# Optimization experiments

Measured on AMD Instinct MI355X. Metric: run time of the kernel, lower is better.

The kernel has to match this reference:

```python
import jax, jax.numpy as jnp
import numpy as np

N, E, F_IN, G = 100000, 1600000, 128, 64
H1, H2, H3 = 64, 32, 16


def _xavier(key, fan_in, fan_out):
    lim = np.sqrt(6.0 / (fan_in + fan_out))
    return jax.random.uniform(key, (fan_in, fan_out), jnp.float32, -lim, lim)


def setup_inputs() -> dict:
    key = jax.random.key(0)
    ks = jax.random.split(key, 16)
    x = jax.random.normal(ks[0], (N, F_IN), jnp.float32)
    edge_index = jax.random.randint(ks[1], (2, E), 0, N, dtype=jnp.int32)
    batch = jnp.sort(jax.random.randint(ks[2], (N,), 0, G, dtype=jnp.int32))
    d = {
        "x": x,
        "W1": _xavier(ks[3], F_IN, H1), "b1": jnp.zeros((H1,), jnp.float32),
        "W2": _xavier(ks[4], H1, H2), "b2": jnp.zeros((H2,), jnp.float32),
        "W3": _xavier(ks[5], H2, H3), "b3": jnp.zeros((H3,), jnp.float32),
        "g1": jnp.ones((H1,), jnp.float32), "be1": jnp.zeros((H1,), jnp.float32),
        "g2": jnp.ones((H2,), jnp.float32), "be2": jnp.zeros((H2,), jnp.float32),
        "g3": jnp.ones((H3,), jnp.float32), "be3": jnp.zeros((H3,), jnp.float32),
        "attn_w": _xavier(ks[6], 3 * H3, 3), "attn_b": jnp.zeros((3,), jnp.float32),
        "fc1_w": _xavier(ks[7], H3, H3), "fc1_b": jnp.zeros((H3,), jnp.float32),
        "fc2_w": _xavier(ks[8], H3, H3 // 2), "fc2_b": jnp.zeros((H3 // 2,), jnp.float32),
        "out_w": _xavier(ks[9], H3 // 2, 1), "out_b": jnp.zeros((1,), jnp.float32),
        "edge_index": edge_index,
        "batch": batch,
        "num_graphs": G,
    }
    return d


def _lrelu(z):
    return jnp.where(z > 0, z, 0.1 * z)


def _bn(h, gamma, beta, eps=1e-5):
    # BatchNorm1d forward with batch statistics (biased variance), as torch training-mode math
    m = jnp.mean(h, axis=0)
    v = jnp.mean(jnp.square(h - m), axis=0)
    return (h - m) * jax.lax.rsqrt(v + eps) * gamma + beta


def reference(x, W1, b1, W2, b2, W3, b3, g1, be1, g2, be2, g3, be3,
              attn_w, attn_b, fc1_w, fc1_b, fc2_w, fc2_b, out_w, out_b,
              edge_index, batch, num_graphs):
    src, dst = edge_index[0], edge_index[1]
    n = x.shape[0]
    # GCN degree with self-loops: deg[i] = 1 + #incoming edges
    deg = jax.ops.segment_sum(jnp.ones((src.shape[0],), x.dtype), dst, num_segments=n) + 1.0
    dis = jax.lax.rsqrt(deg)                      # deg^-1/2, [N]
    enorm = dis[src] * dis[dst]                   # per-edge norm, [E]
    selfw = dis * dis                             # self-loop norm, [N]

    def gcn(h, W, b):
        hw = h @ W                                # [N, H]
        agg = jax.ops.segment_sum(hw[src] * enorm[:, None], dst, num_segments=n)
        return agg + selfw[:, None] * hw + b

    x1 = _lrelu(_bn(gcn(x, W1, b1), g1, be1))     # dropout = identity (eval)
    x2 = _lrelu(_bn(gcn(x1, W2, b2), g2, be2))    # residual skipped: 64 != 32
    x3 = _lrelu(_bn(gcn(x2, W3, b3), g3, be3))    # residual skipped: 32 != 16

    # multi-pool over graphs
    ones_n = jnp.ones((n,), x.dtype)
    counts = jax.ops.segment_sum(ones_n, batch, num_segments=num_graphs)  # [G]
    x_sum = jax.ops.segment_sum(x3, batch, num_segments=num_graphs)       # [G, H3]
    x_mean = x_sum / jnp.maximum(counts, 1.0)[:, None]
    x_max = jax.ops.segment_max(x3, batch, num_segments=num_graphs)

    pooled = jnp.concatenate([x_mean, x_max, x_sum], axis=1)              # [G, 3*H3]
    aw = jax.nn.softmax(pooled @ attn_w + attn_b, axis=1)                 # [G, 3]
    xg = aw[:, 0:1] * x_mean + aw[:, 1:2] * x_max + aw[:, 2:3] * x_sum    # [G, H3]

    xg = _lrelu(xg @ fc1_w + fc1_b)
    xg = _lrelu(xg @ fc2_w + fc2_b)
    out = jax.nn.sigmoid(xg @ out_w + out_b)                              # [G, 1]
    return out
```

## Files before the change

### kernel.cpp

```cpp
#include <hip/hip_runtime.h>

#define GG 64
#define SREP 32
typedef unsigned long long ull;
typedef unsigned short u16;

__device__ __forceinline__ u16 f2b(float x) {
    unsigned u = __float_as_uint(x);
    return (u16)((u + 0x7FFFu + ((u >> 16) & 1u)) >> 16);
}

__device__ __forceinline__ void add8(const uint4 q, float* acc) {
    acc[0] += __uint_as_float(q.x << 16);
    acc[1] += __uint_as_float(q.x & 0xFFFF0000u);
    acc[2] += __uint_as_float(q.y << 16);
    acc[3] += __uint_as_float(q.y & 0xFFFF0000u);
    acc[4] += __uint_as_float(q.z << 16);
    acc[5] += __uint_as_float(q.z & 0xFFFF0000u);
    acc[6] += __uint_as_float(q.w << 16);
    acc[7] += __uint_as_float(q.w & 0xFFFF0000u);
}

__global__ void k_hist(const int* __restrict__ dst, int* __restrict__ cnt, int E) {
    int e = blockIdx.x * blockDim.x + threadIdx.x;
    if (e < E) atomicAdd(&cnt[dst[e]], 1);
}

__global__ void k_dis(const int* __restrict__ cnt, float* __restrict__ dis, int n) {
    int i = blockIdx.x * blockDim.x + threadIdx.x;
    if (i < n) dis[i] = rsqrtf((float)cnt[i] + 1.0f);
}

__global__ void k_scanA(const int* __restrict__ cnt, int* __restrict__ rp,
                        int* __restrict__ bsum, int n) {
    __shared__ int s[256];
    int i = blockIdx.x * 256 + threadIdx.x;
    int v = (i < n) ? cnt[i] : 0;
    s[threadIdx.x] = v;
    __syncthreads();
    for (int off = 1; off < 256; off <<= 1) {
        int t = (threadIdx.x >= off) ? s[threadIdx.x - off] : 0;
        __syncthreads();
        s[threadIdx.x] += t;
        __syncthreads();
    }
    if (i < n) rp[i] = s[threadIdx.x] - v;
    if (threadIdx.x == 255) bsum[blockIdx.x] = s[255];
}

__global__ void k_scanB(int* __restrict__ bsum, int nb) {
    __shared__ int s[512];
    int v = (threadIdx.x < nb) ? bsum[threadIdx.x] : 0;
    s[threadIdx.x] = v;
    __syncthreads();
    for (int off = 1; off < 512; off <<= 1) {
        int t = (threadIdx.x >= off) ? s[threadIdx.x - off] : 0;
        __syncthreads();
        s[threadIdx.x] += t;
        __syncthreads();
    }
    if (threadIdx.x < nb) bsum[threadIdx.x] = s[threadIdx.x] - v;
}

__global__ void k_scanC(int* __restrict__ rp, const int* __restrict__ bsum,
                        int* __restrict__ cursor, int n, int E) {
    int i = blockIdx.x * 256 + threadIdx.x;
    if (i < n) {
        int r = rp[i] + bsum[blockIdx.x];
        rp[i] = r;
        cursor[i] = r;
    }
    if (i == 0) rp[n] = E;
}

__global__ __launch_bounds__(256) void k_scatter(const int* __restrict__ src,
                                                 const int* __restrict__ dst,
                                                 int* __restrict__ cursor,
                                                 ull* __restrict__ epack, int E, int n) {
    const int part = blockIdx.x & 7;
    const int nblk = gridDim.x >> 3;
    const int bser = blockIdx.x >> 3;
    const int lo = (int)(((long long)part * n) >> 3);
    const int hi = (part == 7) ? n : (int)(((long long)(part + 1) * n) >> 3);
    for (int e = bser * 256 + threadIdx.x; e < E; e += nblk * 256) {
        int d = dst[e];
        if (d >= lo && d < hi) {
            int s = src[e];
            int pos = atomicAdd(&cursor[d], 1);
            epack[pos] = (ull)(unsigned)s;
        }
    }
}

template <int FIN, int FOUT, bool BN>
__global__ __launch_bounds__(256) void k_mm(const float* __restrict__ h,
                                            const float* __restrict__ W,
                                            const float* __restrict__ dis,
                                            const float* __restrict__ stats,
                                            const float* __restrict__ gma,
                                            const float* __restrict__ bta,
                                            u16* __restrict__ hw, int n) {
    constexpr int FX  = FOUT / 4;
    constexpr int TY  = 256 / FX;
    constexpr int NT  = TY * 4;
    constexpr int LDA = FIN + ((FOUT == 64) ? 2 : 1);
    __shared__ float sA[NT * LDA];
    __shared__ float sW[FIN * FOUT];
    __shared__ float sSc[FIN], sSh[FIN];

    if (BN && threadIdx.x < FIN) {
        int f = threadIdx.x;
        float s = 0.f, q = 0.f;
        #pragma unroll 8
        for (int r = 0; r < SREP; ++r) {
            s += stats[(r << 7) + f];
            q += stats[(r << 7) + 64 + f];
        }
        float inv_n = 1.0f / (float)n;
        float m = s * inv_n;
        float var = fmaxf(q * inv_n - m * m, 0.f);
        float sc = rsqrtf(var + 1e-5f) * gma[f];
        sSc[f] = sc;
        sSh[f] = bta[f] - m * sc;
    }
    for (int i = threadIdx.x; i < FIN * FOUT / 4; i += 256)
        ((float4*)sW)[i] = ((const float4*)W)[i];
    if (BN) __syncthreads();

    const int node0 = blockIdx.x * NT;
    constexpr int LD4 = NT * FIN / 4 / 256;
    #pragma unroll
    for (int i = 0; i < LD4; ++i) {
        int idx4 = i * 256 + threadIdx.x;
        int row = idx4 / (FIN / 4);
        int c4  = idx4 % (FIN / 4);
        int gn  = node0 + row;
        float4 v = make_float4(0.f, 0.f, 0.f, 0.f);
        if (gn < n) v = ((const float4*)(h + (long long)gn * FIN))[c4];
        if (BN) {
            int f = c4 * 4;
            float t;
            t = fmaf(v.x, sSc[f + 0], sSh[f + 0]); v.x = t > 0.f ? t : 0.1f * t;
            t = fmaf(v.y, sSc[f + 1], sSh[f + 1]); v.y = t > 0.f ? t : 0.1f * t;
            t = fmaf(v.z, sSc[f + 2], sSh[f + 2]); v.z = t > 0.f ? t : 0.1f * t;
            t = fmaf(v.w, sSc[f + 3], sSh[f + 3]); v.w = t > 0.f ? t : 0.1f * t;
        }
        float* p = &sA[row * LDA + c4 * 4];
        p[0] = v.x; p[1] = v.y; p[2] = v.z; p[3] = v.w;
    }
    __syncthreads();

    const int tx = threadIdx.x % FX;
    const int ty = threadIdx.x / FX;
    float acc[4][4];
    #pragma unroll
    for (int i = 0; i < 4; ++i)
        #pragma unroll
        for (int j = 0; j < 4; ++j) acc[i][j] = 0.f;

    #pragma unroll 8
    for (int k = 0; k < FIN; ++k) {
        float4 wv = *((const float4*)&sW[k * FOUT + tx * 4]);
        float a0 = sA[(ty * 4 + 0) * LDA + k];
        float a1 = sA[(ty * 4 + 1) * LDA + k];
        float a2 = sA[(ty * 4 + 2) * LDA + k];
        float a3 = sA[(ty * 4 + 3) * LDA + k];
        acc[0][0] = fmaf(a0, wv.x, acc[0][0]); acc[0][1] = fmaf(a0, wv.y, acc[0][1]);
        acc[0][2] = fmaf(a0, wv.z, acc[0][2]); acc[0][3] = fmaf(a0, wv.w, acc[0][3]);
        acc[1][0] = fmaf(a1, wv.x, acc[1][0]); acc[1][1] = fmaf(a1, wv.y, acc[1][1]);
        acc[1][2] = fmaf(a1, wv.z, acc[1][2]); acc[1][3] = fmaf(a1, wv.w, acc[1][3]);
        acc[2][0] = fmaf(a2, wv.x, acc[2][0]); acc[2][1] = fmaf(a2, wv.y, acc[2][1]);
        acc[2][2] = fmaf(a2, wv.z, acc[2][2]); acc[2][3] = fmaf(a2, wv.w, acc[2][3]);
        acc[3][0] = fmaf(a3, wv.x, acc[3][0]); acc[3][1] = fmaf(a3, wv.y, acc[3][1]);
        acc[3][2] = fmaf(a3, wv.z, acc[3][2]); acc[3][3] = fmaf(a3, wv.w, acc[3][3]);
    }

    #pragma unroll
    for (int i = 0; i < 4; ++i) {
        int gn = node0 + ty * 4 + i;
        if (gn < n) {
            float dv = dis[gn];
            ushort4 o;
            o.x = f2b(acc[i][0] * dv); o.y = f2b(acc[i][1] * dv);
            o.z = f2b(acc[i][2] * dv); o.w = f2b(acc[i][3] * dv);
            ((ushort4*)(hw + (long long)gn * FOUT))[tx] = o;
        }
    }
}

template <int FOUT>
__global__ __launch_bounds__(256) void k_agg(const u16* __restrict__ hwb,
                                             const ull* __restrict__ epack,
                                             const int* __restrict__ rp,
                                             const float* __restrict__ dis,
                                             const float* __restrict__ bias,
                                             float* __restrict__ y,
                                             float* __restrict__ stats, int n) {
    constexpr int LPN = FOUT / 8;
    constexpr int NPB = 256 / LPN;
    constexpr int RS  = FOUT / 8;
    __shared__ float ssum[FOUT], ssq[FOUT];
    for (int i = threadIdx.x; i < FOUT; i += 256) { ssum[i] = 0.f; ssq[i] = 0.f; }
    __syncthreads();
    const int local = threadIdx.x / LPN;
    const int fq = threadIdx.x % LPN;
    const uint4* hw4 = (const uint4*)hwb;
    float b8[8];
    #pragma unroll
    for (int i = 0; i < 8; ++i) b8[i] = bias[fq * 8 + i];
    float lsum[8] = {0,0,0,0,0,0,0,0}, lsq[8] = {0,0,0,0,0,0,0,0};

    int node = blockIdx.x * NPB + local;
    if (node < n) {
        int j0 = rp[node], j1 = rp[node + 1];
        float acc[8] = {0,0,0,0,0,0,0,0};
        int j = j0;
        for (; j + 8 <= j1; j += 8) {
            int s0 = (int)(unsigned)epack[j + 0];
            int s1 = (int)(unsigned)epack[j + 1];
            int s2 = (int)(unsigned)epack[j + 2];
            int s3 = (int)(unsigned)epack[j + 3];
            int s4 = (int)(unsigned)epack[j + 4];
            int s5 = (int)(unsigned)epack[j + 5];
            int s6 = (int)(unsigned)epack[j + 6];
            int s7 = (int)(unsigned)epack[j + 7];
            uint4 q0 = hw4[(long long)s0 * RS + fq];
            uint4 q1 = hw4[(long long)s1 * RS + fq];
            uint4 q2 = hw4[(long long)s2 * RS + fq];
            uint4 q3 = hw4[(long long)s3 * RS + fq];
            uint4 q4 = hw4[(long long)s4 * RS + fq];
            uint4 q5 = hw4[(long long)s5 * RS + fq];
            uint4 q6 = hw4[(long long)s6 * RS + fq];
            uint4 q7 = hw4[(long long)s7 * RS + fq];
            add8(q0, acc); add8(q1, acc); add8(q2, acc); add8(q3, acc);
            add8(q4, acc); add8(q5, acc); add8(q6, acc); add8(q7, acc);
        }
        for (; j + 2 <= j1; j += 2) {
            int s0 = (int)(unsigned)epack[j + 0];
            int s1 = (int)(unsigned)epack[j + 1];
            uint4 q0 = hw4[(long long)s0 * RS + fq];
            uint4 q1 = hw4[(long long)s1 * RS + fq];
            add8(q0, acc); add8(q1, acc);
        }
        for (; j < j1; ++j) {
            uint4 q = hw4[(long long)(unsigned)epack[j] * RS + fq];
            add8(q, acc);
        }
        uint4 qs = hw4[(long long)node * RS + fq];
        add8(qs, acc);
        float dv = dis[node];
        #pragma unroll
        for (int i = 0; i < 8; ++i) acc[i] = fmaf(dv, acc[i], b8[i]);
        float4* y4 = (float4*)y;
        long long o = (long long)node * (FOUT / 4) + fq * 2;
        y4[o]     = make_float4(acc[0], acc[1], acc[2], acc[3]);
        y4[o + 1] = make_float4(acc[4], acc[5], acc[6], acc[7]);
        #pragma unroll
        for (int i = 0; i < 8; ++i) {
            lsum[i] += acc[i];
            lsq[i] = fmaf(acc[i], acc[i], lsq[i]);
        }
    }
    #pragma unroll
    for (int i = 0; i < 8; ++i) {
        atomicAdd(&ssum[fq * 8 + i], lsum[i]);
        atomicAdd(&ssq[fq * 8 + i], lsq[i]);
    }
    __syncthreads();
    float* st = stats + ((blockIdx.x & (SREP - 1)) << 7);
    for (int i = threadIdx.x; i < FOUT; i += 256) {
        atomicAdd(&st[i], ssum[i]);
        atomicAdd(&st[64 + i], ssq[i]);
    }
}

__global__ void k_pool_graph(const float* __restrict__ yraw, const int* __restrict__ batch,
                             const float* __restrict__ stats, const float* __restrict__ gma,
                             const float* __restrict__ bta, int n,
                             float* __restrict__ psum, float* __restrict__ pmax,
                             float* __restrict__ pcnt) {
    const int g = blockIdx.x;
    const int f = threadIdx.x & 15;
    float s = 0.f, q = 0.f;
    #pragma unroll 8
    for (int r = 0; r < SREP; ++r) {
        s += stats[(r << 7) + f];
        q += stats[(r << 7) + 64 + f];
    }
    float inv_n = 1.0f / (float)n;
    float m = s * inv_n;
    float var = fmaxf(q * inv_n - m * m, 0.f);
    float sc = rsqrtf(var + 1e-5f) * gma[f];
    float sh = bta[f] - m * sc;

    __shared__ int s_lo, s_hi;
    if (threadIdx.x == 0) {
        int lo = 0, hi = n;
        while (lo < hi) { int mid = (lo + hi) >> 1; if (batch[mid] < g) lo = mid + 1; else hi = mid; }
        s_lo = lo;
        hi = n;
        while (lo < hi) { int mid = (lo + hi) >> 1; if (batch[mid] < g + 1) lo = mid + 1; else hi = mid; }
        s_hi = lo;
    }
    __syncthreads();
    const int start = s_lo, end = s_hi;
    float lsum = 0.f, lmax = -3.0e38f;
    for (long long idx = (long long)start * 16 + threadIdx.x; idx < (long long)end * 16; idx += blockDim.x) {
        float t = fmaf(yraw[idx], sc, sh);
        float v = t > 0.f ? t : 0.1f * t;
        lsum += v;
        lmax = fmaxf(lmax, v);
    }
    __shared__ float ss[256], sm[256];
    ss[threadIdx.x] = lsum; sm[threadIdx.x] = lmax;
    __syncthreads();
    for (int off = 128; off >= 16; off >>= 1) {
        if (threadIdx.x < off) {
            ss[threadIdx.x] += ss[threadIdx.x + off];
            sm[threadIdx.x] = fmaxf(sm[threadIdx.x], sm[threadIdx.x + off]);
        }
        __syncthreads();
    }
    if (threadIdx.x < 16) {
        psum[g * 16 + threadIdx.x] = ss[threadIdx.x];
        pmax[g * 16 + threadIdx.x] = sm[threadIdx.x];
    }
    if (threadIdx.x == 0) pcnt[g] = (float)(end - start);
}

__global__ void k_head(const float* __restrict__ psum, const float* __restrict__ pmax,
                       const float* __restrict__ pcnt,
                       const float* __restrict__ attn_w, const float* __restrict__ attn_b,
                       const float* __restrict__ fc1_w, const float* __restrict__ fc1_b,
                       const float* __restrict__ fc2_w, const float* __restrict__ fc2_b,
                       const float* __restrict__ out_w, const float* __restrict__ out_b,
                       float* __restrict__ out) {
    int g = threadIdx.x;
    if (g >= GG) return;
    float xs[16], xm[16], xx[16];
    float c = fmaxf(pcnt[g], 1.0f);
    for (int f = 0; f < 16; ++f) {
        xs[f] = psum[(g << 4) + f];
        xm[f] = xs[f] / c;
        xx[f] = pmax[(g << 4) + f];
    }
    float lg[3];
    for (int cI = 0; cI < 3; ++cI) {
        float a = attn_b[cI];
        for (int f = 0; f < 16; ++f) {
            a += xm[f] * attn_w[f * 3 + cI];
            a += xx[f] * attn_w[(16 + f) * 3 + cI];
            a += xs[f] * attn_w[(32 + f) * 3 + cI];
        }
        lg[cI] = a;
    }
    float mx = fmaxf(lg[0], fmaxf(lg[1], lg[2]));
    float e0 = expf(lg[0] - mx), e1 = expf(lg[1] - mx), e2 = expf(lg[2] - mx);
    float inv = 1.0f / (e0 + e1 + e2);
    float a0 = e0 * inv, a1 = e1 * inv, a2 = e2 * inv;
    float xg[16];
    for (int f = 0; f < 16; ++f) xg[f] = a0 * xm[f] + a1 * xx[f] + a2 * xs[f];
    float t1[16];
    for (int j = 0; j < 16; ++j) {
        float a = fc1_b[j];
        for (int k = 0; k < 16; ++k) a += xg[k] * fc1_w[k * 16 + j];
        t1[j] = a > 0.f ? a : 0.1f * a;
    }
    float t2[8];
    for (int j = 0; j < 8; ++j) {
        float a = fc2_b[j];
        for (int k = 0; k < 16; ++k) a += t1[k] * fc2_w[k * 8 + j];
        t2[j] = a > 0.f ? a : 0.1f * a;
    }
    float o = out_b[0];
    for (int k = 0; k < 8; ++k) o += t2[k] * out_w[k];
    o = 1.0f / (1.0f + expf(-o));
    out[g] = o;
}

extern "C" void kernel_launch(void* const* d_in, const int* in_sizes, int n_in,
                              void* d_out, int out_size, void* d_ws, size_t ws_size,
                              hipStream_t stream) {
    const float* x      = (const float*)d_in[0];
    const float* W1     = (const float*)d_in[1];  const float* b1   = (const float*)d_in[2];
    const float* W2     = (const float*)d_in[3];  const float* b2   = (const float*)d_in[4];
    const float* W3     = (const float*)d_in[5];  const float* b3   = (const float*)d_in[6];
    const float* g1     = (const float*)d_in[7];  const float* be1  = (const float*)d_in[8];
    const float* g2     = (const float*)d_in[9];  const float* be2  = (const float*)d_in[10];
    const float* g3     = (const float*)d_in[11]; const float* be3  = (const float*)d_in[12];
    const float* attn_w = (const float*)d_in[13]; const float* attn_b = (const float*)d_in[14];
    const float* fc1_w  = (const float*)d_in[15]; const float* fc1_b  = (const float*)d_in[16];
    const float* fc2_w  = (const float*)d_in[17]; const float* fc2_b  = (const float*)d_in[18];
    const float* out_w  = (const float*)d_in[19]; const float* out_b  = (const float*)d_in[20];
    const int* edge_index = (const int*)d_in[21];
    const int* batch      = (const int*)d_in[22];

    const int N = in_sizes[0] / 128;
    const int E = in_sizes[21] / 2;
    const int* srcp = edge_index;
    const int* dstp = edge_index + E;
    const int nb = (N + 255) / 256;

    char* ws = (char*)d_ws;
    float* dis    = (float*)(ws);
    int*   cnt    = (int*)(ws + 0x80000);
    int*   rp     = (int*)(ws + 0x100000);
    int*   bsum   = (int*)(ws + 0x180000);
    float* stats1 = (float*)(ws + 0x180800);
    float* stats2 = (float*)(ws + 0x184800);
    float* stats3 = (float*)(ws + 0x188800);
    float* psum   = (float*)(ws + 0x18C800);
    float* pmax   = (float*)(ws + 0x18D800);
    float* pcnt   = (float*)(ws + 0x18E800);
    ull*   epack  = (ull*)(ws + 0x190000);
    float* buf1   = (float*)(ws + 0x190000 + (size_t)E * 8);
    u16*   hwb    = (u16*)(buf1 + (size_t)N * 64);

    hipMemsetAsync(cnt, 0, (size_t)N * 4, stream);
    k_hist<<<(E + 255) / 256, 256, 0, stream>>>(dstp, cnt, E);
    k_dis<<<nb, 256, 0, stream>>>(cnt, dis, N);
    k_scanA<<<nb, 256, 0, stream>>>(cnt, rp, bsum, N);
    k_scanB<<<1, 512, 0, stream>>>(bsum, nb);
    k_scanC<<<nb, 256, 0, stream>>>(rp, bsum, cnt, N, E);
    k_scatter<<<2048, 256, 0, stream>>>(srcp, dstp, cnt, epack, E, N);
    hipMemsetAsync(stats1, 0, 3 * SREP * 512, stream);

    const int gr1 = (N + 31) / 32;
    const int gr2 = (N + 63) / 64;
    const int gr3 = (N + 127) / 128;

    k_mm<128, 64, false><<<(N + 63) / 64, 256, 0, stream>>>(
        x, W1, dis, nullptr, nullptr, nullptr, hwb, N);
    k_agg<64><<<gr1, 256, 0, stream>>>(hwb, epack, rp, dis, b1, buf1, stats1, N);

    k_mm<64, 32, true><<<(N + 127) / 128, 256, 0, stream>>>(
        buf1, W2, dis, stats1, g1, be1, hwb, N);
    k_agg<32><<<gr2, 256, 0, stream>>>(hwb, epack, rp, dis, b2, buf1, stats2, N);

    k_mm<32, 16, true><<<(N + 255) / 256, 256, 0, stream>>>(
        buf1, W3, dis, stats2, g2, be2, hwb, N);
    k_agg<16><<<gr3, 256, 0, stream>>>(hwb, epack, rp, dis, b3, buf1, stats3, N);

    k_pool_graph<<<GG, 256, 0, stream>>>(buf1, batch, stats3, g3, be3, N, psum, pmax, pcnt);
    k_head<<<1, 64, 0, stream>>>(psum, pmax, pcnt, attn_w, attn_b,
                                 fc1_w, fc1_b, fc2_w, fc2_b, out_w, out_b,
                                 (float*)d_out);
}
```

Measured before the change: 579.3 us.

## Bucket CSR edges by source range and aggregate bucket-by-bucket for cache locality

Edges are now sub-sorted per destination into 8 source-index buckets of 16K nodes each, using per-(node,bucket) histograms and cursors. A new aggregation kernel walks all nodes' bucket 0 edges, then bucket 1, and so on, so concurrent gathers touch a narrower slice of the hw feature table and hit cache more often. Edge storage also shrinks from 64-bit to 32-bit indices. In exchange the CSR build does 8x more counter work, bucket loops add per-node overhead and shorter inner runs, and only the first two layers use the new kernel.

```diff
diff --git a/kernel.cpp b/kernel.cpp
--- a/kernel.cpp
+++ b/kernel.cpp
@@ -2,8 +2,10 @@
 
 #define GG 64
 #define SREP 32
+#define BSH 14
 typedef unsigned long long ull;
 typedef unsigned short u16;
+typedef unsigned int uint;
 
 __device__ __forceinline__ u16 f2b(float x) {
     unsigned u = __float_as_uint(x);
@@ -21,14 +23,25 @@
     acc[7] += __uint_as_float(q.w & 0xFFFF0000u);
 }
 
-__global__ void k_hist(const int* __restrict__ dst, int* __restrict__ cnt, int E) {
+__global__ void k_hist(const int* __restrict__ src, const int* __restrict__ dst,
+                       int* __restrict__ cnt4, int E) {
     int e = blockIdx.x * blockDim.x + threadIdx.x;
-    if (e < E) atomicAdd(&cnt[dst[e]], 1);
-}
-
-__global__ void k_dis(const int* __restrict__ cnt, float* __restrict__ dis, int n) {
+    if (e < E) {
+        int b = min(src[e] >> BSH, 7);
+        atomicAdd(&cnt4[(dst[e] << 3) + b], 1);
+    }
+}
+
+__global__ void k_sum4(const int* __restrict__ cnt4, int* __restrict__ cnt,
+                       float* __restrict__ dis, int n) {
     int i = blockIdx.x * blockDim.x + threadIdx.x;
-    if (i < n) dis[i] = rsqrtf((float)cnt[i] + 1.0f);
+    if (i < n) {
+        int t = 0;
+        #pragma unroll
+        for (int b = 0; b < 8; ++b) t += cnt4[(i << 3) + b];
+        cnt[i] = t;
+        dis[i] = rsqrtf((float)t + 1.0f);
+    }
 }
 
 __global__ void k_scanA(const int* __restrict__ cnt, int* __restrict__ rp,
@@ -63,20 +76,26 @@
 }
 
 __global__ void k_scanC(int* __restrict__ rp, const int* __restrict__ bsum,
-                        int* __restrict__ cursor, int n, int E) {
+                        const int* __restrict__ cnt4, int* __restrict__ cursor4,
+                        int n, int E) {
     int i = blockIdx.x * 256 + threadIdx.x;
     if (i < n) {
         int r = rp[i] + bsum[blockIdx.x];
         rp[i] = r;
-        cursor[i] = r;
+        int run = r;
+        #pragma unroll
+        for (int b = 0; b < 8; ++b) {
+            cursor4[(i << 3) + b] = run;
+            run += cnt4[(i << 3) + b];
+        }
     }
     if (i == 0) rp[n] = E;
 }
 
 __global__ __launch_bounds__(256) void k_scatter(const int* __restrict__ src,
                                                  const int* __restrict__ dst,
-                                                 int* __restrict__ cursor,
-                                                 ull* __restrict__ epack, int E, int n) {
+                                                 int* __restrict__ cursor4,
+                                                 uint* __restrict__ epack, int E, int n) {
     const int part = blockIdx.x & 7;
     const int nblk = gridDim.x >> 3;
     const int bser = blockIdx.x >> 3;
@@ -86,8 +105,9 @@
         int d = dst[e];
         if (d >= lo && d < hi) {
             int s = src[e];
-            int pos = atomicAdd(&cursor[d], 1);
-            epack[pos] = (ull)(unsigned)s;
+            int b = min(s >> BSH, 7);
+            int pos = atomicAdd(&cursor4[(d << 3) + b], 1);
+            epack[pos] = (uint)s;
         }
     }
 }
@@ -188,9 +208,104 @@
     }
 }
 
+template <int FOUT, int NPG>
+__global__ __launch_bounds__(256) void k_aggb(const u16* __restrict__ hwb,
+                                              const uint* __restrict__ epack,
+                                              const int* __restrict__ rp,
+                                              const int* __restrict__ cursor4,
+                                              const float* __restrict__ dis,
+                                              const float* __restrict__ bias,
+                                              float* __restrict__ y,
+                                              float* __restrict__ stats,
+                                              int n, int nbuck) {
+    constexpr int LPN = FOUT / 8;
+    constexpr int GPB = 256 / LPN;
+    constexpr int NPB = GPB * NPG;
+    constexpr int RS  = FOUT / 8;
+    __shared__ float ssum[FOUT], ssq[FOUT];
+    for (int i = threadIdx.x; i < FOUT; i += 256) { ssum[i] = 0.f; ssq[i] = 0.f; }
+    __syncthreads();
+    const int grp = threadIdx.x / LPN;
+    const int fq  = threadIdx.x % LPN;
+    const uint4* hw4 = (const uint4*)hwb;
+
+    float acc[NPG][8];
+    int nd[NPG];
+    #pragma unroll
+    for (int t = 0; t < NPG; ++t) {
+        nd[t] = blockIdx.x * NPB + grp * NPG + t;
+        #pragma unroll
+        for (int i = 0; i < 8; ++i) acc[t][i] = 0.f;
+    }
+
+    for (int b = 0; b < nbuck; ++b) {
+        #pragma unroll
+        for (int t = 0; t < NPG; ++t) {
+            int node = nd[t];
+            if (node < n) {
+                int j0 = (b == 0) ? rp[node] : cursor4[(node << 3) + b - 1];
+                int j1 = cursor4[(node << 3) + b];
+                int j = j0;
+                for (; j + 4 <= j1; j += 4) {
+                    uint s0 = epack[j + 0];
+                    uint s1 = epack[j + 1];
+                    uint s2 = epack[j + 2];
+                    uint s3 = epack[j + 3];
+                    uint4 q0 = hw4[(long long)s0 * RS + fq];
+                    uint4 q1 = hw4[(long long)s1 * RS + fq];
+                    uint4 q2 = hw4[(long long)s2 * RS + fq];
+                    uint4 q3 = hw4[(long long)s3 * RS + fq];
+                    add8(q0, acc[t]); add8(q1, acc[t]);
+                    add8(q2, acc[t]); add8(q3, acc[t]);
+                }
+                for (; j < j1; ++j) {
+                    uint4 q = hw4[(long long)epack[j] * RS + fq];
+                    add8(q, acc[t]);
+                }
+            }
+        }
+    }
+
+    float lsum[8] = {0,0,0,0,0,0,0,0}, lsq[8] = {0,0,0,0,0,0,0,0};
+    float b8[8];
+    #pragma unroll
+    for (int i = 0; i < 8; ++i) b8[i] = bias[fq * 8 + i];
+    #pragma unroll
+    for (int t = 0; t < NPG; ++t) {
+        int node = nd[t];
+        if (node < n) {
+            uint4 qs = hw4[(long long)node * RS + fq];
+            add8(qs, acc[t]);
+            float dv = dis[node];
+            #pragma unroll
+            for (int i = 0; i < 8; ++i) acc[t][i] = fmaf(dv, acc[t][i], b8[i]);
+            float4* y4 = (float4*)y;
+            long long o = (long long)node * (FOUT / 4) + fq * 2;
+            y4[o]     = make_float4(acc[t][0], acc[t][1], acc[t][2], acc[t][3]);
+            y4[o + 1] = make_float4(acc[t][4], acc[t][5], acc[t][6], acc[t][7]);
+            #pragma unroll
+            for (int i = 0; i < 8; ++i) {
+                lsum[i] += acc[t][i];
+                lsq[i] = fmaf(acc[t][i], acc[t][i], lsq[i]);
+            }
+        }
+    }
+    #pragma unroll
+    for (int i = 0; i < 8; ++i) {
+        atomicAdd(&ssum[fq * 8 + i], lsum[i]);
+        atomicAdd(&ssq[fq * 8 + i], lsq[i]);
+    }
+    __syncthreads();
+    float* st = stats + ((blockIdx.x & (SREP - 1)) << 7);
+    for (int i = threadIdx.x; i < FOUT; i += 256) {
+        atomicAdd(&st[i], ssum[i]);
+        atomicAdd(&st[64 + i], ssq[i]);
+    }
+}
+
 template <int FOUT>
 __global__ __launch_bounds__(256) void k_agg(const u16* __restrict__ hwb,
-                                             const ull* __restrict__ epack,
+                                             const uint* __restrict__ epack,
                                              const int* __restrict__ rp,
                                              const float* __restrict__ dis,
                                              const float* __restrict__ bias,
@@ -216,14 +331,8 @@
         float acc[8] = {0,0,0,0,0,0,0,0};
         int j = j0;
         for (; j + 8 <= j1; j += 8) {
-            int s0 = (int)(unsigned)epack[j + 0];
-            int s1 = (int)(unsigned)epack[j + 1];
-            int s2 = (int)(unsigned)epack[j + 2];
-            int s3 = (int)(unsigned)epack[j + 3];
-            int s4 = (int)(unsigned)epack[j + 4];
-            int s5 = (int)(unsigned)epack[j + 5];
-            int s6 = (int)(unsigned)epack[j + 6];
-            int s7 = (int)(unsigned)epack[j + 7];
+            uint s0 = epack[j + 0], s1 = epack[j + 1], s2 = epack[j + 2], s3 = epack[j + 3];
+            uint s4 = epack[j + 4], s5 = epack[j + 5], s6 = epack[j + 6], s7 = epack[j + 7];
             uint4 q0 = hw4[(long long)s0 * RS + fq];
             uint4 q1 = hw4[(long long)s1 * RS + fq];
             uint4 q2 = hw4[(long long)s2 * RS + fq];
@@ -236,14 +345,13 @@
             add8(q4, acc); add8(q5, acc); add8(q6, acc); add8(q7, acc);
         }
         for (; j + 2 <= j1; j += 2) {
-            int s0 = (int)(unsigned)epack[j + 0];
-            int s1 = (int)(unsigned)epack[j + 1];
+            uint s0 = epack[j + 0], s1 = epack[j + 1];
             uint4 q0 = hw4[(long long)s0 * RS + fq];
             uint4 q1 = hw4[(long long)s1 * RS + fq];
             add8(q0, acc); add8(q1, acc);
         }
         for (; j < j1; ++j) {
-            uint4 q = hw4[(long long)(unsigned)epack[j] * RS + fq];
+            uint4 q = hw4[(long long)epack[j] * RS + fq];
             add8(q, acc);
         }
         uint4 qs = hw4[(long long)node * RS + fq];
@@ -400,6 +508,7 @@
     const int* srcp = edge_index;
     const int* dstp = edge_index + E;
     const int nb = (N + 255) / 256;
+    const int NBUCK = min((N + (1 << BSH) - 1) >> BSH, 8);
 
     char* ws = (char*)d_ws;
     float* dis    = (float*)(ws);
@@ -412,34 +521,34 @@
     float* psum   = (float*)(ws + 0x18C800);
     float* pmax   = (float*)(ws + 0x18D800);
     float* pcnt   = (float*)(ws + 0x18E800);
-    ull*   epack  = (ull*)(ws + 0x190000);
-    float* buf1   = (float*)(ws + 0x190000 + (size_t)E * 8);
-    u16*   hwb    = (u16*)(buf1 + (size_t)N * 64);
-
-    hipMemsetAsync(cnt, 0, (size_t)N * 4, stream);
-    k_hist<<<(E + 255) / 256, 256, 0, stream>>>(dstp, cnt, E);
-    k_dis<<<nb, 256, 0, stream>>>(cnt, dis, N);
+    int*   cnt4    = (int*)(ws + 0x190000);
+    int*   cursor4 = cnt4 + (size_t)8 * N;
+    uint*  epack   = (uint*)(cursor4 + (size_t)8 * N);
+    float* buf1    = (float*)((char*)epack + (((size_t)E * 4 + 255) & ~(size_t)255));
+    u16*   hwb     = (u16*)(buf1 + (size_t)N * 64);
+
+    hipMemsetAsync(cnt4, 0, (size_t)N * 32, stream);
+    k_hist<<<(E + 255) / 256, 256, 0, stream>>>(srcp, dstp, cnt4, E);
+    k_sum4<<<nb, 256, 0, stream>>>(cnt4, cnt, dis, N);
     k_scanA<<<nb, 256, 0, stream>>>(cnt, rp, bsum, N);
     k_scanB<<<1, 512, 0, stream>>>(bsum, nb);
-    k_scanC<<<nb, 256, 0, stream>>>(rp, bsum, cnt, N, E);
-    k_scatter<<<2048, 256, 0, stream>>>(srcp, dstp, cnt, epack, E, N);
+    k_scanC<<<nb, 256, 0, stream>>>(rp, bsum, cnt4, cursor4, N, E);
+    k_scatter<<<2048, 256, 0, stream>>>(srcp, dstp, cursor4, epack, E, N);
     hipMemsetAsync(stats1, 0, 3 * SREP * 512, stream);
-
-    const int gr1 = (N + 31) / 32;
-    const int gr2 = (N + 63) / 64;
-    const int gr3 = (N + 127) / 128;
 
     k_mm<128, 64, false><<<(N + 63) / 64, 256, 0, stream>>>(
         x, W1, dis, nullptr, nullptr, nullptr, hwb, N);
-    k_agg<64><<<gr1, 256, 0, stream>>>(hwb, epack, rp, dis, b1, buf1, stats1, N);
+    k_aggb<64, 2><<<(N + 63) / 64, 256, 0, stream>>>(
+        hwb, epack, rp, cursor4, dis, b1, buf1, stats1, N, NBUCK);
 
     k_mm<64, 32, true><<<(N + 127) / 128, 256, 0, stream>>>(
         buf1, W2, dis, stats1, g1, be1, hwb, N);
-    k_agg<32><<<gr2, 256, 0, stream>>>(hwb, epack, rp, dis, b2, buf1, stats2, N);
+    k_aggb<32, 1><<<(N + 63) / 64, 256, 0, stream>>>(
+        hwb, epack, rp, cursor4, dis, b2, buf1, stats2, N, NBUCK);
 
     k_mm<32, 16, true><<<(N + 255) / 256, 256, 0, stream>>>(
         buf1, W3, dis, stats2, g2, be2, hwb, N);
-    k_agg<16><<<gr3, 256, 0, stream>>>(hwb, epack, rp, dis, b3, buf1, stats3, N);
+    k_agg<16><<<(N + 127) / 128, 256, 0, stream>>>(hwb, epack, rp, dis, b3, buf1, stats3, N);
 
     k_pool_graph<<<GG, 256, 0, stream>>>(buf1, batch, stats3, g3, be3, N, psum, pmax, pcnt);
     k_head<<<1, 64, 0, stream>>>(psum, pmax, pcnt, attn_w, attn_b,
```

New measurement: 561.7 us. 3.0% less time.

## Bucket edges by dst-block and src-range; aggregate via shared-memory atomics

Applied to the files above, without the earlier changes.

Replaces the per-node CSR with segments keyed by (64-node destination block, 8K-node source bucket), packing the source id and local destination into one 32-bit word. Each aggregation block processes all edges of its 64 destination nodes in source-sorted order and accumulates into an LDS tile with atomics that are rotated by lane to reduce bank conflicts. The aim is better cache locality for the gathered rows, better load balance than one thread-group per node, and half the edge-array bytes. The cost is many LDS atomic adds per edge, a larger scan over segments, and an extra histogram atomic.

```diff
diff --git a/kernel.cpp b/kernel.cpp
--- a/kernel.cpp
+++ b/kernel.cpp
@@ -2,8 +2,10 @@
 
 #define GG 64
 #define SREP 32
+#define BSH 13
 typedef unsigned long long ull;
 typedef unsigned short u16;
+typedef unsigned int uint;
 
 __device__ __forceinline__ u16 f2b(float x) {
     unsigned u = __float_as_uint(x);
@@ -21,9 +23,27 @@
     acc[7] += __uint_as_float(q.w & 0xFFFF0000u);
 }
 
-__global__ void k_hist(const int* __restrict__ dst, int* __restrict__ cnt, int E) {
+__device__ __forceinline__ void upk8(const uint4 q, float* f) {
+    f[0] = __uint_as_float(q.x << 16);
+    f[1] = __uint_as_float(q.x & 0xFFFF0000u);
+    f[2] = __uint_as_float(q.y << 16);
+    f[3] = __uint_as_float(q.y & 0xFFFF0000u);
+    f[4] = __uint_as_float(q.z << 16);
+    f[5] = __uint_as_float(q.z & 0xFFFF0000u);
+    f[6] = __uint_as_float(q.w << 16);
+    f[7] = __uint_as_float(q.w & 0xFFFF0000u);
+}
+
+__global__ void k_hist(const int* __restrict__ src, const int* __restrict__ dst,
+                       int* __restrict__ cnt, int* __restrict__ segcnt,
+                       int E, int nbuck) {
     int e = blockIdx.x * blockDim.x + threadIdx.x;
-    if (e < E) atomicAdd(&cnt[dst[e]], 1);
+    if (e < E) {
+        int d = dst[e];
+        atomicAdd(&cnt[d], 1);
+        int b = min(src[e] >> BSH, nbuck - 1);
+        atomicAdd(&segcnt[(d >> 6) * nbuck + b], 1);
+    }
 }
 
 __global__ void k_dis(const int* __restrict__ cnt, float* __restrict__ dis, int n) {
@@ -62,21 +82,22 @@
     if (threadIdx.x < nb) bsum[threadIdx.x] = s[threadIdx.x] - v;
 }
 
-__global__ void k_scanC(int* __restrict__ rp, const int* __restrict__ bsum,
-                        int* __restrict__ cursor, int n, int E) {
+__global__ void k_scanC(int* __restrict__ segstart, const int* __restrict__ bsum,
+                        int* __restrict__ segcur, int nseg, int E) {
     int i = blockIdx.x * 256 + threadIdx.x;
-    if (i < n) {
-        int r = rp[i] + bsum[blockIdx.x];
-        rp[i] = r;
-        cursor[i] = r;
-    }
-    if (i == 0) rp[n] = E;
+    if (i < nseg) {
+        int r = segstart[i] + bsum[blockIdx.x];
+        segstart[i] = r;
+        segcur[i] = r;
+    }
+    if (i == 0) segstart[nseg] = E;
 }
 
 __global__ __launch_bounds__(256) void k_scatter(const int* __restrict__ src,
                                                  const int* __restrict__ dst,
-                                                 int* __restrict__ cursor,
-                                                 ull* __restrict__ epack, int E, int n) {
+                                                 int* __restrict__ segcur,
+                                                 uint* __restrict__ epack,
+                                                 int E, int n, int nbuck) {
     const int part = blockIdx.x & 7;
     const int nblk = gridDim.x >> 3;
     const int bser = blockIdx.x >> 3;
@@ -86,8 +107,10 @@
         int d = dst[e];
         if (d >= lo && d < hi) {
             int s = src[e];
-            int pos = atomicAdd(&cursor[d], 1);
-            epack[pos] = (ull)(unsigned)s;
+            int b = min(s >> BSH, nbuck - 1);
+            int seg = (d >> 6) * nbuck + b;
+            int pos = atomicAdd(&segcur[seg], 1);
+            epack[pos] = (uint)s | ((uint)(d & 63) << 26);
         }
     }
 }
@@ -189,82 +212,87 @@
 }
 
 template <int FOUT>
-__global__ __launch_bounds__(256) void k_agg(const u16* __restrict__ hwb,
-                                             const ull* __restrict__ epack,
-                                             const int* __restrict__ rp,
-                                             const float* __restrict__ dis,
-                                             const float* __restrict__ bias,
-                                             float* __restrict__ y,
-                                             float* __restrict__ stats, int n) {
-    constexpr int LPN = FOUT / 8;
-    constexpr int NPB = 256 / LPN;
-    constexpr int RS  = FOUT / 8;
+__device__ __forceinline__ void lds_acc(float* acc, uint u, int fq, const uint4 q) {
+    int dl = (int)(u >> 26);
+    float f[8];
+    upk8(q, f);
+    int base = dl * FOUT + fq * 8;
+    #pragma unroll
+    for (int i = 0; i < 8; ++i)
+        atomicAdd(&acc[base + ((i + dl) & 7)], f[i]);
+}
+
+template <int FOUT>
+__global__ __launch_bounds__(256) void k_agge(const u16* __restrict__ hwb,
+                                              const uint* __restrict__ epack,
+                                              const int* __restrict__ segstart,
+                                              const float* __restrict__ dis,
+                                              const float* __restrict__ bias,
+                                              float* __restrict__ y,
+                                              float* __restrict__ stats,
+                                              int n, int nbuck) {
+    constexpr int LPN   = FOUT / 8;
+    constexpr int SLOTS = 256 / LPN;
+    constexpr int RS    = FOUT / 8;
+    __shared__ float acc[64 * FOUT];
     __shared__ float ssum[FOUT], ssq[FOUT];
+    for (int i = threadIdx.x; i < 64 * FOUT; i += 256) acc[i] = 0.f;
     for (int i = threadIdx.x; i < FOUT; i += 256) { ssum[i] = 0.f; ssq[i] = 0.f; }
     __syncthreads();
-    const int local = threadIdx.x / LPN;
-    const int fq = threadIdx.x % LPN;
+
+    const int slot = threadIdx.x / LPN;
+    const int fq   = threadIdx.x % LPN;
     const uint4* hw4 = (const uint4*)hwb;
-    float b8[8];
-    #pragma unroll
-    for (int i = 0; i < 8; ++i) b8[i] = bias[fq * 8 + i];
-    float lsum[8] = {0,0,0,0,0,0,0,0}, lsq[8] = {0,0,0,0,0,0,0,0};
-
-    int node = blockIdx.x * NPB + local;
-    if (node < n) {
-        int j0 = rp[node], j1 = rp[node + 1];
-        float acc[8] = {0,0,0,0,0,0,0,0};
-        int j = j0;
-        for (; j + 8 <= j1; j += 8) {
-            int s0 = (int)(unsigned)epack[j + 0];
-            int s1 = (int)(unsigned)epack[j + 1];
-            int s2 = (int)(unsigned)epack[j + 2];
-            int s3 = (int)(unsigned)epack[j + 3];
-            int s4 = (int)(unsigned)epack[j + 4];
-            int s5 = (int)(unsigned)epack[j + 5];
-            int s6 = (int)(unsigned)epack[j + 6];
-            int s7 = (int)(unsigned)epack[j + 7];
-            uint4 q0 = hw4[(long long)s0 * RS + fq];
-            uint4 q1 = hw4[(long long)s1 * RS + fq];
-            uint4 q2 = hw4[(long long)s2 * RS + fq];
-            uint4 q3 = hw4[(long long)s3 * RS + fq];
-            uint4 q4 = hw4[(long long)s4 * RS + fq];
-            uint4 q5 = hw4[(long long)s5 * RS + fq];
-            uint4 q6 = hw4[(long long)s6 * RS + fq];
-            uint4 q7 = hw4[(long long)s7 * RS + fq];
-            add8(q0, acc); add8(q1, acc); add8(q2, acc); add8(q3, acc);
-            add8(q4, acc); add8(q5, acc); add8(q6, acc); add8(q7, acc);
-        }
-        for (; j + 2 <= j1; j += 2) {
-            int s0 = (int)(unsigned)epack[j + 0];
-            int s1 = (int)(unsigned)epack[j + 1];
-            uint4 q0 = hw4[(long long)s0 * RS + fq];
-            uint4 q1 = hw4[(long long)s1 * RS + fq];
-            add8(q0, acc); add8(q1, acc);
-        }
-        for (; j < j1; ++j) {
-            uint4 q = hw4[(long long)(unsigned)epack[j] * RS + fq];
-            add8(q, acc);
-        }
-        uint4 qs = hw4[(long long)node * RS + fq];
-        add8(qs, acc);
-        float dv = dis[node];
-        #pragma unroll
-        for (int i = 0; i < 8; ++i) acc[i] = fmaf(dv, acc[i], b8[i]);
-        float4* y4 = (float4*)y;
-        long long o = (long long)node * (FOUT / 4) + fq * 2;
-        y4[o]     = make_float4(acc[0], acc[1], acc[2], acc[3]);
-        y4[o + 1] = make_float4(acc[4], acc[5], acc[6], acc[7]);
-        #pragma unroll
-        for (int i = 0; i < 8; ++i) {
-            lsum[i] += acc[i];
-            lsq[i] = fmaf(acc[i], acc[i], lsq[i]);
-        }
-    }
-    #pragma unroll
-    for (int i = 0; i < 8; ++i) {
-        atomicAdd(&ssum[fq * 8 + i], lsum[i]);
-        atomicAdd(&ssq[fq * 8 + i], lsq[i]);
+    const int J0 = segstart[blockIdx.x * nbuck];
+    const int J1 = segstart[blockIdx.x * nbuck + nbuck];
+
+    int j = J0 + slot;
+    for (; j + 3 * SLOTS < J1; j += 4 * SLOTS) {
+        uint u0 = epack[j];
+        uint u1 = epack[j + SLOTS];
+        uint u2 = epack[j + 2 * SLOTS];
+        uint u3 = epack[j + 3 * SLOTS];
+        uint4 q0 = hw4[(long long)(u0 & 0x3FFFFFFu) * RS + fq];
+        uint4 q1 = hw4[(long long)(u1 & 0x3FFFFFFu) * RS + fq];
+        uint4 q2 = hw4[(long long)(u2 & 0x3FFFFFFu) * RS + fq];
+        uint4 q3 = hw4[(long long)(u3 & 0x3FFFFFFu) * RS + fq];
+        lds_acc<FOUT>(acc, u0, fq, q0);
+        lds_acc<FOUT>(acc, u1, fq, q1);
+        lds_acc<FOUT>(acc, u2, fq, q2);
+        lds_acc<FOUT>(acc, u3, fq, q3);
+    }
+    for (; j < J1; j += SLOTS) {
+        uint u = epack[j];
+        uint4 q = hw4[(long long)(u & 0x3FFFFFFu) * RS + fq];
+        lds_acc<FOUT>(acc, u, fq, q);
+    }
+    __syncthreads();
+
+    constexpr int UNITS = 64 * LPN;
+    for (int u = threadIdx.x; u < UNITS; u += 256) {
+        int nd   = u / LPN;
+        int fqe  = u % LPN;
+        int node = blockIdx.x * 64 + nd;
+        if (node < n) {
+            float f[8];
+            int base = nd * FOUT + fqe * 8;
+            #pragma unroll
+            for (int i = 0; i < 8; ++i) f[i] = acc[base + ((i + nd) & 7)];
+            uint4 qs = hw4[(long long)node * RS + fqe];
+            add8(qs, f);
+            float dv = dis[node];
+            #pragma unroll
+            for (int i = 0; i < 8; ++i) f[i] = fmaf(dv, f[i], bias[fqe * 8 + i]);
+            float4* y4 = (float4*)y;
+            long long o = (long long)node * (FOUT / 4) + fqe * 2;
+            y4[o]     = make_float4(f[0], f[1], f[2], f[3]);
+            y4[o + 1] = make_float4(f[4], f[5], f[6], f[7]);
+            #pragma unroll
+            for (int i = 0; i < 8; ++i) {
+                atomicAdd(&ssum[fqe * 8 + i], f[i]);
+                atomicAdd(&ssq[fqe * 8 + i], f[i] * f[i]);
+            }
+        }
     }
     __syncthreads();
     float* st = stats + ((blockIdx.x & (SREP - 1)) << 7);
@@ -400,46 +428,48 @@
     const int* srcp = edge_index;
     const int* dstp = edge_index + E;
     const int nb = (N + 255) / 256;
+    const int NBUCK = min((N + (1 << BSH) - 1) >> BSH, 32);
+    const int NBLK  = (N + 63) / 64;
+    const int NSEG  = NBLK * NBUCK;
+    const int nbseg = (NSEG + 255) / 256;
 
     char* ws = (char*)d_ws;
-    float* dis    = (float*)(ws);
-    int*   cnt    = (int*)(ws + 0x80000);
-    int*   rp     = (int*)(ws + 0x100000);
-    int*   bsum   = (int*)(ws + 0x180000);
-    float* stats1 = (float*)(ws + 0x180800);
-    float* stats2 = (float*)(ws + 0x184800);
-    float* stats3 = (float*)(ws + 0x188800);
-    float* psum   = (float*)(ws + 0x18C800);
-    float* pmax   = (float*)(ws + 0x18D800);
-    float* pcnt   = (float*)(ws + 0x18E800);
-    ull*   epack  = (ull*)(ws + 0x190000);
-    float* buf1   = (float*)(ws + 0x190000 + (size_t)E * 8);
-    u16*   hwb    = (u16*)(buf1 + (size_t)N * 64);
-
-    hipMemsetAsync(cnt, 0, (size_t)N * 4, stream);
-    k_hist<<<(E + 255) / 256, 256, 0, stream>>>(dstp, cnt, E);
+    float* dis      = (float*)(ws);
+    int*   cnt      = (int*)(ws + 0x80000);
+    int*   segcnt   = (int*)(ws + 0x100000);
+    int*   segstart = (int*)(ws + 0x120000);
+    int*   segcur   = (int*)(ws + 0x140000);
+    int*   bsum     = (int*)(ws + 0x160000);
+    float* stats1   = (float*)(ws + 0x161000);
+    float* stats2   = (float*)(ws + 0x165000);
+    float* stats3   = (float*)(ws + 0x169000);
+    float* psum     = (float*)(ws + 0x16D000);
+    float* pmax     = (float*)(ws + 0x16E000);
+    float* pcnt     = (float*)(ws + 0x16F000);
+    uint*  epack    = (uint*)(ws + 0x170000);
+    float* buf1     = (float*)(ws + 0x170000 + (((size_t)E * 4 + 255) & ~(size_t)255));
+    u16*   hwb      = (u16*)(buf1 + (size_t)N * 64);
+
+    hipMemsetAsync(cnt, 0, 0x80000 + (size_t)NSEG * 4, stream);
+    k_hist<<<(E + 255) / 256, 256, 0, stream>>>(srcp, dstp, cnt, segcnt, E, NBUCK);
     k_dis<<<nb, 256, 0, stream>>>(cnt, dis, N);
-    k_scanA<<<nb, 256, 0, stream>>>(cnt, rp, bsum, N);
-    k_scanB<<<1, 512, 0, stream>>>(bsum, nb);
-    k_scanC<<<nb, 256, 0, stream>>>(rp, bsum, cnt, N, E);
-    k_scatter<<<2048, 256, 0, stream>>>(srcp, dstp, cnt, epack, E, N);
+    k_scanA<<<nbseg, 256, 0, stream>>>(segcnt, segstart, bsum, NSEG);
+    k_scanB<<<1, 512, 0, stream>>>(bsum, nbseg);
+    k_scanC<<<nbseg, 256, 0, stream>>>(segstart, bsum, segcur, NSEG, E);
+    k_scatter<<<2048, 256, 0, stream>>>(srcp, dstp, segcur, epack, E, N, NBUCK);
     hipMemsetAsync(stats1, 0, 3 * SREP * 512, stream);
-
-    const int gr1 = (N + 31) / 32;
-    const int gr2 = (N + 63) / 64;
-    const int gr3 = (N + 127) / 128;
 
     k_mm<128, 64, false><<<(N + 63) / 64, 256, 0, stream>>>(
         x, W1, dis, nullptr, nullptr, nullptr, hwb, N);
-    k_agg<64><<<gr1, 256, 0, stream>>>(hwb, epack, rp, dis, b1, buf1, stats1, N);
+    k_agge<64><<<NBLK, 256, 0, stream>>>(hwb, epack, segstart, dis, b1, buf1, stats1, N, NBUCK);
 
     k_mm<64, 32, true><<<(N + 127) / 128, 256, 0, stream>>>(
         buf1, W2, dis, stats1, g1, be1, hwb, N);
-    k_agg<32><<<gr2, 256, 0, stream>>>(hwb, epack, rp, dis, b2, buf1, stats2, N);
+    k_agge<32><<<NBLK, 256, 0, stream>>>(hwb, epack, segstart, dis, b2, buf1, stats2, N, NBUCK);
 
     k_mm<32, 16, true><<<(N + 255) / 256, 256, 0, stream>>>(
         buf1, W3, dis, stats2, g2, be2, hwb, N);
-    k_agg<16><<<gr3, 256, 0, stream>>>(hwb, epack, rp, dis, b3, buf1, stats3, N);
+    k_agge<16><<<NBLK, 256, 0, stream>>>(hwb, epack, segstart, dis, b3, buf1, stats3, N, NBUCK);
 
     k_pool_graph<<<GG, 256, 0, stream>>>(buf1, batch, stats3, g3, be3, N, psum, pmax, pcnt);
     k_head<<<1, 64, 0, stream>>>(psum, pmax, pcnt, attn_w, attn_b,
```

Result: slower. 1.633 ms (+181.9%).

## Bucket CSR neighbors by source range and shrink edge indices to 32-bit

Applied to the files above, without the earlier changes.

The histogram and scatter now keep 8 per-destination sub-counters keyed by source-index range (src>>14), so each node's neighbor list comes out roughly ordered by source. This is meant to improve gather locality in the aggregation kernels. The edge array shrinks from 64-bit to 32-bit entries, halving its traffic, and the aggregation unroll drops from 8 to 4. In exchange there are 8x larger count and cursor arrays, an extra memset, and heavier scan and scatter kernels. The smaller unroll also leaves fewer loads in flight per thread.

```diff
diff --git a/kernel.cpp b/kernel.cpp
--- a/kernel.cpp
+++ b/kernel.cpp
@@ -2,8 +2,10 @@
 
 #define GG 64
 #define SREP 32
+#define BSH 14
 typedef unsigned long long ull;
 typedef unsigned short u16;
+typedef unsigned int uint;
 
 __device__ __forceinline__ u16 f2b(float x) {
     unsigned u = __float_as_uint(x);
@@ -21,14 +23,25 @@
     acc[7] += __uint_as_float(q.w & 0xFFFF0000u);
 }
 
-__global__ void k_hist(const int* __restrict__ dst, int* __restrict__ cnt, int E) {
+__global__ void k_hist(const int* __restrict__ src, const int* __restrict__ dst,
+                       int* __restrict__ cnt4, int E) {
     int e = blockIdx.x * blockDim.x + threadIdx.x;
-    if (e < E) atomicAdd(&cnt[dst[e]], 1);
-}
-
-__global__ void k_dis(const int* __restrict__ cnt, float* __restrict__ dis, int n) {
+    if (e < E) {
+        int b = min(src[e] >> BSH, 7);
+        atomicAdd(&cnt4[(dst[e] << 3) + b], 1);
+    }
+}
+
+__global__ void k_sum4(const int* __restrict__ cnt4, int* __restrict__ cnt,
+                       float* __restrict__ dis, int n) {
     int i = blockIdx.x * blockDim.x + threadIdx.x;
-    if (i < n) dis[i] = rsqrtf((float)cnt[i] + 1.0f);
+    if (i < n) {
+        int t = 0;
+        #pragma unroll
+        for (int b = 0; b < 8; ++b) t += cnt4[(i << 3) + b];
+        cnt[i] = t;
+        dis[i] = rsqrtf((float)t + 1.0f);
+    }
 }
 
 __global__ void k_scanA(const int* __restrict__ cnt, int* __restrict__ rp,
@@ -63,20 +76,26 @@
 }
 
 __global__ void k_scanC(int* __restrict__ rp, const int* __restrict__ bsum,
-                        int* __restrict__ cursor, int n, int E) {
+                        const int* __restrict__ cnt4, int* __restrict__ cursor4,
+                        int n, int E) {
     int i = blockIdx.x * 256 + threadIdx.x;
     if (i < n) {
         int r = rp[i] + bsum[blockIdx.x];
         rp[i] = r;
-        cursor[i] = r;
+        int run = r;
+        #pragma unroll
+        for (int b = 0; b < 8; ++b) {
+            cursor4[(i << 3) + b] = run;
+            run += cnt4[(i << 3) + b];
+        }
     }
     if (i == 0) rp[n] = E;
 }
 
 __global__ __launch_bounds__(256) void k_scatter(const int* __restrict__ src,
                                                  const int* __restrict__ dst,
-                                                 int* __restrict__ cursor,
-                                                 ull* __restrict__ epack, int E, int n) {
+                                                 int* __restrict__ cursor4,
+                                                 uint* __restrict__ epack, int E, int n) {
     const int part = blockIdx.x & 7;
     const int nblk = gridDim.x >> 3;
     const int bser = blockIdx.x >> 3;
@@ -86,8 +105,9 @@
         int d = dst[e];
         if (d >= lo && d < hi) {
             int s = src[e];
-            int pos = atomicAdd(&cursor[d], 1);
-            epack[pos] = (ull)(unsigned)s;
+            int b = min(s >> BSH, 7);
+            int pos = atomicAdd(&cursor4[(d << 3) + b], 1);
+            epack[pos] = (uint)s;
         }
     }
 }
@@ -190,7 +210,7 @@
 
 template <int FOUT>
 __global__ __launch_bounds__(256) void k_agg(const u16* __restrict__ hwb,
-                                             const ull* __restrict__ epack,
+                                             const uint* __restrict__ epack,
                                              const int* __restrict__ rp,
                                              const float* __restrict__ dis,
                                              const float* __restrict__ bias,
@@ -215,35 +235,17 @@
         int j0 = rp[node], j1 = rp[node + 1];
         float acc[8] = {0,0,0,0,0,0,0,0};
         int j = j0;
-        for (; j + 8 <= j1; j += 8) {
-            int s0 = (int)(unsigned)epack[j + 0];
-            int s1 = (int)(unsigned)epack[j + 1];
-            int s2 = (int)(unsigned)epack[j + 2];
-            int s3 = (int)(unsigned)epack[j + 3];
-            int s4 = (int)(unsigned)epack[j + 4];
-            int s5 = (int)(unsigned)epack[j + 5];
-            int s6 = (int)(unsigned)epack[j + 6];
-            int s7 = (int)(unsigned)epack[j + 7];
+        for (; j + 4 <= j1; j += 4) {
+            uint s0 = epack[j + 0], s1 = epack[j + 1];
+            uint s2 = epack[j + 2], s3 = epack[j + 3];
             uint4 q0 = hw4[(long long)s0 * RS + fq];
             uint4 q1 = hw4[(long long)s1 * RS + fq];
             uint4 q2 = hw4[(long long)s2 * RS + fq];
             uint4 q3 = hw4[(long long)s3 * RS + fq];
-            uint4 q4 = hw4[(long long)s4 * RS + fq];
-            uint4 q5 = hw4[(long long)s5 * RS + fq];
-            uint4 q6 = hw4[(long long)s6 * RS + fq];
-            uint4 q7 = hw4[(long long)s7 * RS + fq];
             add8(q0, acc); add8(q1, acc); add8(q2, acc); add8(q3, acc);
-            add8(q4, acc); add8(q5, acc); add8(q6, acc); add8(q7, acc);
-        }
-        for (; j + 2 <= j1; j += 2) {
-            int s0 = (int)(unsigned)epack[j + 0];
-            int s1 = (int)(unsigned)epack[j + 1];
-            uint4 q0 = hw4[(long long)s0 * RS + fq];
-            uint4 q1 = hw4[(long long)s1 * RS + fq];
-            add8(q0, acc); add8(q1, acc);
         }
         for (; j < j1; ++j) {
-            uint4 q = hw4[(long long)(unsigned)epack[j] * RS + fq];
+            uint4 q = hw4[(long long)epack[j] * RS + fq];
             add8(q, acc);
         }
         uint4 qs = hw4[(long long)node * RS + fq];
@@ -412,17 +414,19 @@
     float* psum   = (float*)(ws + 0x18C800);
     float* pmax   = (float*)(ws + 0x18D800);
     float* pcnt   = (float*)(ws + 0x18E800);
-    ull*   epack  = (ull*)(ws + 0x190000);
-    float* buf1   = (float*)(ws + 0x190000 + (size_t)E * 8);
-    u16*   hwb    = (u16*)(buf1 + (size_t)N * 64);
-
-    hipMemsetAsync(cnt, 0, (size_t)N * 4, stream);
-    k_hist<<<(E + 255) / 256, 256, 0, stream>>>(dstp, cnt, E);
-    k_dis<<<nb, 256, 0, stream>>>(cnt, dis, N);
+    int*   cnt4    = (int*)(ws + 0x190000);
+    int*   cursor4 = cnt4 + (size_t)8 * N;
+    uint*  epack   = (uint*)(cursor4 + (size_t)8 * N);
+    float* buf1    = (float*)((char*)epack + (((size_t)E * 4 + 255) & ~(size_t)255));
+    u16*   hwb     = (u16*)(buf1 + (size_t)N * 64);
+
+    hipMemsetAsync(cnt4, 0, (size_t)N * 32, stream);
+    k_hist<<<(E + 255) / 256, 256, 0, stream>>>(srcp, dstp, cnt4, E);
+    k_sum4<<<nb, 256, 0, stream>>>(cnt4, cnt, dis, N);
     k_scanA<<<nb, 256, 0, stream>>>(cnt, rp, bsum, N);
     k_scanB<<<1, 512, 0, stream>>>(bsum, nb);
-    k_scanC<<<nb, 256, 0, stream>>>(rp, bsum, cnt, N, E);
-    k_scatter<<<2048, 256, 0, stream>>>(srcp, dstp, cnt, epack, E, N);
+    k_scanC<<<nb, 256, 0, stream>>>(rp, bsum, cnt4, cursor4, N, E);
+    k_scatter<<<2048, 256, 0, stream>>>(srcp, dstp, cursor4, epack, E, N);
     hipMemsetAsync(stats1, 0, 3 * SREP * 512, stream);
 
     const int gr1 = (N + 31) / 32;
```

New measurement: 571.2 us. About the same (-1.4%).
